# Kernel optimization log

Measured on AMD Instinct MI355X. Metric: run time of the kernel, lower is better.

The kernel has to match this reference:

```python
import jax, jax.numpy as jnp
import numpy as np

B, T, E, H, D = 4, 1024, 1024, 16, 64


def rel_shift(x):
    # x: [B, H, T1, T2] -> Transformer-XL relative shift
    b, h, t1, t2 = x.shape
    x = jnp.pad(x, ((0, 0), (0, 0), (0, 0), (1, 0)))  # pad zeros on left of last dim
    x = x.reshape(b, h, t2 + 1, t1)[:, :, 1:]
    return x.reshape(b, h, t1, t2)


def setup_inputs() -> dict:
    key = jax.random.key(0)
    ks = jax.random.split(key, 9)
    s = 0.02
    return {
        "x": jax.random.normal(ks[0], (B, T, E), jnp.float32),
        "pos": jax.random.normal(ks[1], (1, T, E), jnp.float32),
        "Wq": jax.random.normal(ks[2], (E, H, D), jnp.float32) * s,
        "Wk": jax.random.normal(ks[3], (E, H, D), jnp.float32) * s,
        "Wv": jax.random.normal(ks[4], (E, H, D), jnp.float32) * s,
        "Wr": jax.random.normal(ks[5], (E, H, D), jnp.float32) * s,
        "r_w_bias": jax.random.normal(ks[6], (1, H, 1, D), jnp.float32) * s,
        "r_r_bias": jax.random.normal(ks[7], (1, H, 1, D), jnp.float32) * s,
        "merge_W": jax.random.normal(ks[8], (E, E), jnp.float32) * s,
        "merge_b": jnp.zeros((E,), jnp.float32),
    }


def reference(x, pos, Wq, Wk, Wv, Wr, r_w_bias, r_r_bias, merge_W, merge_b):
    d = Wq.shape[-1]
    scale = d ** -0.5
    # per-head linear projections via einsum (MultiHeadLinear)
    q = jnp.einsum('bte,ehd->bhtd', x, Wq) * scale   # [B,H,T,D]
    k = jnp.einsum('bte,ehd->bhtd', x, Wk)           # [B,H,T,D]
    v = jnp.einsum('bte,ehd->bhtd', x, Wv)           # [B,H,T,D]
    r = jnp.einsum('upe,ehd->uhpd', pos, Wr)[0]      # [H,P,D], P == T

    # content logits: (q + u) . k
    content_logits = jnp.einsum('bhtd,bhsd->bhts', q + r_w_bias, k)
    # relative logits: (q + v_bias) . rel_keys, then rel_shift
    relative_logits = jnp.einsum('bhtd,hpd->bhtp', q + r_r_bias, r)
    relative_logits = rel_shift(relative_logits)

    logits = content_logits + relative_logits        # [B,H,T,T]
    weights = jax.nn.softmax(logits, axis=-1)
    # attend and merge heads: [B,T,H,D] -> [B,T,E]
    attended = jnp.einsum('bhts,bhsd->bthd', weights, v).reshape(x.shape[0], x.shape[1], -1)
    return attended @ merge_W + merge_b
```

## Files before the change

kernel.cpp:

```cpp
#include <hip/hip_runtime.h>
#include <hip/hip_bf16.h>

#define BB 4
#define TT 1024
#define EE 1024
#define HH 16
#define DD 64

typedef unsigned short ushort_t;
typedef unsigned int uint_t;
typedef __attribute__((ext_vector_type(8))) short short8;
typedef __attribute__((ext_vector_type(4))) float f32x4;

__device__ __forceinline__ ushort_t f2bf(float f) {
  uint_t u = __float_as_uint(f);
  u += 0x7fffu + ((u >> 16) & 1u);
  return (ushort_t)(u >> 16);
}
__device__ __forceinline__ float bf2f(ushort_t s) {
  return __uint_as_float(((uint_t)s) << 16);
}

__device__ __forceinline__ void gload16(const ushort_t* src, ushort_t* dst) {
  __builtin_amdgcn_global_load_lds(
      (const __attribute__((address_space(1))) void*)src,
      (__attribute__((address_space(3))) void*)dst, 16, 0, 0);
}

__global__ void __launch_bounds__(256) conv_flat(
    const float* __restrict__ in, ushort_t* __restrict__ out, int n) {
  int i = (blockIdx.x * 256 + threadIdx.x) * 8;
  if (i >= n) return;
  float4 a = *(const float4*)(in + i);
  float4 b = *(const float4*)(in + i + 4);
  uint4 o;
  o.x = (uint_t)f2bf(a.x) | ((uint_t)f2bf(a.y) << 16);
  o.y = (uint_t)f2bf(a.z) | ((uint_t)f2bf(a.w) << 16);
  o.z = (uint_t)f2bf(b.x) | ((uint_t)f2bf(b.y) << 16);
  o.w = (uint_t)f2bf(b.z) | ((uint_t)f2bf(b.w) << 16);
  *(uint4*)(out + i) = o;
}

__global__ void __launch_bounds__(256) trans_conv(
    const float* __restrict__ W, ushort_t* __restrict__ Oh,
    ushort_t* __restrict__ Ol, int has_lo) {
  __shared__ float Ts[64][65];
  const int n0 = blockIdx.x * 64, k0 = blockIdx.y * 64;
  const int t = threadIdx.x;
  const int r = t >> 2, cs = (t & 3) * 16;
  const float* src = W + (size_t)(k0 + r) * 1024 + n0 + cs;
  #pragma unroll
  for (int e = 0; e < 16; e += 4) {
    float4 v4 = *(const float4*)(src + e);
    Ts[r][cs + e] = v4.x; Ts[r][cs + e + 1] = v4.y;
    Ts[r][cs + e + 2] = v4.z; Ts[r][cs + e + 3] = v4.w;
  }
  __syncthreads();
  ushort_t hb[16], lb[16];
  #pragma unroll
  for (int e = 0; e < 16; e++) {
    float v = Ts[cs + e][r];
    hb[e] = f2bf(v);
    lb[e] = f2bf(v - bf2f(hb[e]));
  }
  ushort_t* dh = Oh + (size_t)(n0 + r) * 1024 + k0 + cs;
  *(uint4*)dh = *(const uint4*)hb;
  *(uint4*)(dh + 8) = *(const uint4*)(hb + 8);
  if (has_lo) {
    ushort_t* dl = Ol + (size_t)(n0 + r) * 1024 + k0 + cs;
    *(uint4*)dl = *(const uint4*)lb;
    *(uint4*)(dl + 8) = *(const uint4*)(lb + 8);
  }
}

__global__ void __launch_bounds__(256) mfma_gemm_proj(
    const ushort_t* __restrict__ A,
    const ushort_t* __restrict__ B0, const ushort_t* __restrict__ B1,
    const ushort_t* __restrict__ B2,
    ushort_t* __restrict__ o_qu, ushort_t* __restrict__ o_qv,
    ushort_t* __restrict__ o_k, ushort_t* __restrict__ o_v,
    const float* __restrict__ bias_u, const float* __restrict__ bias_v,
    int mode) {
  __shared__ ushort_t sA[2][128 * 32];
  __shared__ ushort_t sB[2][128 * 32];
  const int tid = threadIdx.x;
  const int w = tid >> 6, lane = tid & 63, g = lane >> 4, cl = lane & 15;
  const int wr = w >> 1, wc = w & 1;

  int widx, n0l;
  const ushort_t* Bt;
  if (mode == 0) {
    widx = blockIdx.x >> 3;
    n0l = (blockIdx.x & 7) * 128;
    Bt = (widx == 0) ? B0 : ((widx == 1) ? B1 : B2);
  } else {
    widx = 3;
    n0l = blockIdx.x * 128;
    Bt = B0;
  }
  const int m0 = blockIdx.y * 128;

  f32x4 acc[4][4];
  #pragma unroll
  for (int fi = 0; fi < 4; fi++)
    #pragma unroll
    for (int fj = 0; fj < 4; fj++) acc[fi][fj] = (f32x4){0.f, 0.f, 0.f, 0.f};

  auto STAGE = [&](int buf, int t) {
    const int k0b = t * 64;
    #pragma unroll
    for (int i = 0; i < 2; i++) {
      int cb = w * 128 + i * 64;
      int c = cb + lane;
      const char* sa = (const char*)A + (size_t)(m0 + (c >> 2)) * 2048 + k0b + (c & 3) * 16;
      gload16((const ushort_t*)sa, &sA[buf][cb * 8]);
      const char* sb = (const char*)Bt + (size_t)(n0l + (c >> 2)) * 2048 + k0b + (c & 3) * 16;
      gload16((const ushort_t*)sb, &sB[buf][cb * 8]);
    }
  };

  STAGE(0, 0);
  __syncthreads();
  int cur = 0;
  for (int t = 0; t < 32; t++) {
    if (t + 1 < 32) STAGE(cur ^ 1, t + 1);
    short8 af[4], bfr[4];
    #pragma unroll
    for (int f = 0; f < 4; f++) {
      af[f] = *(const short8*)&sA[cur][(wr * 64 + f * 16 + cl) * 32 + g * 8];
      bfr[f] = *(const short8*)&sB[cur][(wc * 64 + f * 16 + cl) * 32 + g * 8];
    }
    #pragma unroll
    for (int fi = 0; fi < 4; fi++)
      #pragma unroll
      for (int fj = 0; fj < 4; fj++)
        acc[fi][fj] = __builtin_amdgcn_mfma_f32_16x16x32_bf16(af[fi], bfr[fj], acc[fi][fj], 0, 0, 0);
    __syncthreads();
    cur ^= 1;
  }

  #pragma unroll
  for (int fi = 0; fi < 4; fi++)
    #pragma unroll
    for (int fj = 0; fj < 4; fj++)
      #pragma unroll
      for (int reg = 0; reg < 4; reg++) {
        int m = m0 + wr * 64 + fi * 16 + 4 * g + reg;
        int n = n0l + wc * 64 + fj * 16 + cl;
        float val = acc[fi][fj][reg];
        int h = n >> 6, d = n & 63;
        if (mode == 0) {
          int b = m >> 10, tt = m & 1023;
          size_t idx = (((size_t)(b * HH + h)) * TT + tt) * DD + d;
          if (widx == 0) {
            float s = val * 0.125f;
            o_qu[idx] = f2bf(s + bias_u[n]);
            o_qv[idx] = f2bf(s + bias_v[n]);
          } else if (widx == 1) {
            o_k[idx] = f2bf(val);
          } else {
            o_v[idx] = f2bf(val);
          }
        } else {
          size_t idx = ((size_t)h * TT + m) * DD + d;
          o_qu[idx] = f2bf(val);
        }
      }
}

__global__ void __launch_bounds__(256) mfma_gemm_merge(
    const ushort_t* __restrict__ Ah, const ushort_t* __restrict__ Al,
    const ushort_t* __restrict__ Bh, const ushort_t* __restrict__ Bl,
    const float* __restrict__ bias, float* __restrict__ out) {
  __shared__ ushort_t sAh[2][128 * 32], sAl[2][128 * 32];
  __shared__ ushort_t sBh[2][128 * 32], sBl[2][128 * 32];
  const int tid = threadIdx.x;
  const int w = tid >> 6, lane = tid & 63, g = lane >> 4, cl = lane & 15;
  const int wr = w >> 1, wc = w & 1;
  const int n0l = blockIdx.x * 128;
  const int m0 = blockIdx.y * 128;

  f32x4 acc[4][4];
  #pragma unroll
  for (int fi = 0; fi < 4; fi++)
    #pragma unroll
    for (int fj = 0; fj < 4; fj++) acc[fi][fj] = (f32x4){0.f, 0.f, 0.f, 0.f};

  auto STAGE = [&](int buf, int t) {
    const int k0b = t * 64;
    #pragma unroll
    for (int i = 0; i < 2; i++) {
      int cb = w * 128 + i * 64;
      int c = cb + lane;
      size_t offA = (size_t)(m0 + (c >> 2)) * 2048 + k0b + (c & 3) * 16;
      size_t offB = (size_t)(n0l + (c >> 2)) * 2048 + k0b + (c & 3) * 16;
      gload16((const ushort_t*)((const char*)Ah + offA), &sAh[buf][cb * 8]);
      gload16((const ushort_t*)((const char*)Al + offA), &sAl[buf][cb * 8]);
      gload16((const ushort_t*)((const char*)Bh + offB), &sBh[buf][cb * 8]);
      gload16((const ushort_t*)((const char*)Bl + offB), &sBl[buf][cb * 8]);
    }
  };

  STAGE(0, 0);
  __syncthreads();
  int cur = 0;
  for (int t = 0; t < 32; t++) {
    if (t + 1 < 32) STAGE(cur ^ 1, t + 1);
    short8 ah[4], al[4], bh[4], bl[4];
    #pragma unroll
    for (int f = 0; f < 4; f++) {
      int ra = (wr * 64 + f * 16 + cl) * 32 + g * 8;
      int rb = (wc * 64 + f * 16 + cl) * 32 + g * 8;
      ah[f] = *(const short8*)&sAh[cur][ra];
      al[f] = *(const short8*)&sAl[cur][ra];
      bh[f] = *(const short8*)&sBh[cur][rb];
      bl[f] = *(const short8*)&sBl[cur][rb];
    }
    #pragma unroll
    for (int fi = 0; fi < 4; fi++)
      #pragma unroll
      for (int fj = 0; fj < 4; fj++) {
        acc[fi][fj] = __builtin_amdgcn_mfma_f32_16x16x32_bf16(ah[fi], bh[fj], acc[fi][fj], 0, 0, 0);
        acc[fi][fj] = __builtin_amdgcn_mfma_f32_16x16x32_bf16(al[fi], bh[fj], acc[fi][fj], 0, 0, 0);
        acc[fi][fj] = __builtin_amdgcn_mfma_f32_16x16x32_bf16(ah[fi], bl[fj], acc[fi][fj], 0, 0, 0);
      }
    __syncthreads();
    cur ^= 1;
  }

  #pragma unroll
  for (int fi = 0; fi < 4; fi++)
    #pragma unroll
    for (int fj = 0; fj < 4; fj++)
      #pragma unroll
      for (int reg = 0; reg < 4; reg++) {
        int m = m0 + wr * 64 + fi * 16 + 4 * g + reg;
        int n = n0l + wc * 64 + fj * 16 + cl;
        out[(size_t)m * 1024 + n] = acc[fi][fj][reg] + bias[n];
      }
}

__device__ __forceinline__ void stage8(ushort_t* region, const ushort_t* grow0,
                                       int r0, int lane, int rmax) {
  int flat16 = r0 * 8 + lane;
  int row = flat16 >> 3;
  int ch = flat16 & 7;
  int gr = row > rmax ? rmax : row;
  const ushort_t* src = grow0 + (size_t)gr * 64 + ((((ch << 4) ^ ((row & 7) << 4))) >> 1);
  gload16(src, region + r0 * 64);
}

__device__ __forceinline__ short8 ldsw(const ushort_t* base, int row, int offB) {
  const char* p = (const char*)base + row * 128 + (offB ^ ((row & 7) << 4));
  return *(const short8*)p;
}

__global__ void __launch_bounds__(256, 3) attn_mfma_kernel(
    const ushort_t* __restrict__ qu_g, const ushort_t* __restrict__ qv_g,
    const ushort_t* __restrict__ k_g, const ushort_t* __restrict__ v_g,
    const ushort_t* __restrict__ r_g,
    ushort_t* __restrict__ att_h, ushort_t* __restrict__ att_l)
{
    __shared__ ushort_t sK[2][64 * 64];
    __shared__ ushort_t sVt[2][64 * 72];
    __shared__ ushort_t sG[4][2304];

    const int tid = threadIdx.x;
    const int w = tid >> 6;
    const int lane = tid & 63;
    const int g = lane >> 4;
    const int cl = lane & 15;

    const int i0 = blockIdx.x * 64;
    const int h = blockIdx.y;
    const int b = blockIdx.z;
    const size_t base_bh = ((size_t)(b * HH + h)) * TT * DD;
    const ushort_t* rh = r_g + (size_t)h * TT * DD;

    ushort_t* Gw = sG[w];
    ushort_t* Pb = sG[w];

    const int qrow = i0 + 16 * w + cl;
    const ushort_t* qup = qu_g + base_bh + (size_t)qrow * 64;
    short8 aQ0 = *(const short8*)(qup + 8 * g);
    short8 aQ1 = *(const short8*)(qup + 32 + 8 * g);
    const ushort_t* qv1p = qv_g + base_bh + (size_t)qrow * 64;
    short8 aV0 = *(const short8*)(qv1p + 8 * g);
    short8 aV1 = *(const short8*)(qv1p + 32 + 8 * g);
    int r2row = qrow + 1; if (r2row > 1023) r2row = 1023;
    const ushort_t* qv2p = qv_g + base_bh + (size_t)r2row * 64;
    short8 aV0s = *(const short8*)(qv2p + 8 * g);
    short8 aV1s = *(const short8*)(qv2p + 32 + 8 * g);

    auto STAGEK = [&](int bufi, int jt16) {
      const ushort_t* kb = k_g + base_bh + (size_t)(jt16 * 64) * 64;
      stage8(sK[bufi], kb, 16 * w, lane, 63);
      stage8(sK[bufi], kb, 16 * w + 8, lane, 63);
    };
    const int vjj = tid & 63;
    const int vd0 = (tid >> 6) * 16;
    auto LOADV = [&](int jt16, short8& v0, short8& v1) {
      const ushort_t* vs = v_g + base_bh + (size_t)(jt16 * 64 + vjj) * 64 + vd0;
      v0 = *(const short8*)vs;
      v1 = *(const short8*)(vs + 8);
    };
    auto WRITEV = [&](int bufi, short8 v0, short8 v1) {
      ushort_t* dst = &sVt[bufi][0];
      #pragma unroll
      for (int e = 0; e < 8; e++) dst[(vd0 + e) * 72 + vjj] = (ushort_t)v0[e];
      #pragma unroll
      for (int e = 0; e < 8; e++) dst[(vd0 + 8 + e) * 72 + vjj] = (ushort_t)v1[e];
    };

    f32x4 Oa[4];
    #pragma unroll
    for (int q = 0; q < 4; q++) Oa[q] = (f32x4){0.f, 0.f, 0.f, 0.f};
    float mrun[4] = {-1e30f, -1e30f, -1e30f, -1e30f};
    float lrun[4] = {0.f, 0.f, 0.f, 0.f};

    STAGEK(0, 0);
    short8 pv0, pv1;
    LOADV(0, pv0, pv1);
    WRITEV(0, pv0, pv1);
    __syncthreads();
    int cur = 0;

    for (int jt16 = 0; jt16 < 16; jt16++) {
        const int j0 = jt16 * 64;
        const int dji = j0 - i0;
        ushort_t* Gw2 = Gw + ((dji == 0) ? 64 * 18 : 0);

        f32x4 sacc[4];
        #pragma unroll
        for (int jt = 0; jt < 4; jt++) sacc[jt] = (f32x4){0.f, 0.f, 0.f, 0.f};
        __builtin_amdgcn_s_setprio(1);
        #pragma unroll
        for (int jt = 0; jt < 4; jt++) {
            int krow = jt * 16 + cl;
            short8 b0 = ldsw(sK[cur], krow, 16 * g);
            short8 b1 = ldsw(sK[cur], krow, 64 + 16 * g);
            sacc[jt] = __builtin_amdgcn_mfma_f32_16x16x32_bf16(aQ0, b0, sacc[jt], 0, 0, 0);
            sacc[jt] = __builtin_amdgcn_mfma_f32_16x16x32_bf16(aQ1, b1, sacc[jt], 0, 0, 0);
        }
        __builtin_amdgcn_s_setprio(0);

        if (dji <= 0) {
            int cbase = 960 + dji;
            int nsub = (dji == 0) ? 4 : 8;
            for (int sub = 0; sub < nsub; sub++) {
                int m = sub * 16 + cl;
                int rr = cbase + m;
                rr = rr < 0 ? 0 : (rr > 1023 ? 1023 : rr);
                const ushort_t* rp = rh + (size_t)rr * 64 + 8 * g;
                f32x4 gacc = (f32x4){0.f, 0.f, 0.f, 0.f};
                gacc = __builtin_amdgcn_mfma_f32_16x16x32_bf16(aV0, *(const short8*)rp, gacc, 0, 0, 0);
                gacc = __builtin_amdgcn_mfma_f32_16x16x32_bf16(aV1, *(const short8*)(rp + 32), gacc, 0, 0, 0);
                *(uint_t*)(Gw + m * 18 + 4 * g) =
                    (uint_t)f2bf(gacc[0]) | ((uint_t)f2bf(gacc[1]) << 16);
                *(uint_t*)(Gw + m * 18 + 4 * g + 2) =
                    (uint_t)f2bf(gacc[2]) | ((uint_t)f2bf(gacc[3]) << 16);
            }
        }
        if (dji >= 0) {
            int cb2 = dji - 65; if (cb2 < 0) cb2 = 0;
            int nsub = (dji == 0) ? 4 : 8;
            for (int sub = 0; sub < nsub; sub++) {
                int m = sub * 16 + cl;
                int rr = cb2 + m;
                rr = rr > 1023 ? 1023 : rr;
                const ushort_t* rp = rh + (size_t)rr * 64 + 8 * g;
                f32x4 gacc = (f32x4){0.f, 0.f, 0.f, 0.f};
                gacc = __builtin_amdgcn_mfma_f32_16x16x32_bf16(aV0s, *(const short8*)rp, gacc, 0, 0, 0);
                gacc = __builtin_amdgcn_mfma_f32_16x16x32_bf16(aV1s, *(const short8*)(rp + 32), gacc, 0, 0, 0);
                *(uint_t*)(Gw2 + m * 18 + 4 * g) =
                    (uint_t)f2bf(gacc[0]) | ((uint_t)f2bf(gacc[1]) << 16);
                *(uint_t*)(Gw2 + m * 18 + 4 * g + 2) =
                    (uint_t)f2bf(gacc[2]) | ((uint_t)f2bf(gacc[3]) << 16);
            }
        }

        if (jt16 + 1 < 16) {
            STAGEK(cur ^ 1, jt16 + 1);
            LOADV(jt16 + 1, pv0, pv1);
        }

        if (dji <= 0) {
            int lim = 63 - dji;
            #pragma unroll
            for (int jt = 0; jt < 4; jt++)
                #pragma unroll
                for (int reg = 0; reg < 4; reg++) {
                    int m1 = 63 + jt * 16 + cl - 16 * w - 4 * g - reg;
                    if (m1 <= lim) sacc[jt][reg] += bf2f(Gw[m1 * 18 + 4 * g + reg]);
                }
        }
        if (dji >= 0) {
            int cb2 = dji - 65; if (cb2 < 0) cb2 = 0;
            #pragma unroll
            for (int jt = 0; jt < 4; jt++)
                #pragma unroll
                for (int reg = 0; reg < 4; reg++) {
                    int dlt = dji + jt * 16 + cl - 16 * w - 4 * g - reg;
                    if (dlt >= 2) sacc[jt][reg] += bf2f(Gw2[(dlt - 2 - cb2) * 18 + 4 * g + reg]);
                }
        }

        #pragma unroll
        for (int reg = 0; reg < 4; reg++) {
            float tmax = fmaxf(fmaxf(sacc[0][reg], sacc[1][reg]),
                               fmaxf(sacc[2][reg], sacc[3][reg]));
            #pragma unroll
            for (int msk = 1; msk <= 8; msk <<= 1) tmax = fmaxf(tmax, __shfl_xor(tmax, msk));
            float mnew = fmaxf(mrun[reg], tmax);
            float sc = __expf(mrun[reg] - mnew);
            mrun[reg] = mnew;
            float psum = 0.f;
            #pragma unroll
            for (int jt = 0; jt < 4; jt++) {
                float p = __expf(sacc[jt][reg] - mnew);
                psum += p;
                Pb[(4 * g + reg) * 72 + jt * 16 + cl] = f2bf(p);
            }
            #pragma unroll
            for (int msk = 1; msk <= 8; msk <<= 1) psum += __shfl_xor(psum, msk);
            lrun[reg] = lrun[reg] * sc + psum;
            #pragma unroll
            for (int q = 0; q < 4; q++) Oa[q][reg] *= sc;
        }

        __builtin_amdgcn_s_setprio(1);
        #pragma unroll
        for (int kk = 0; kk < 2; kk++) {
            short8 aP = *(const short8*)((const char*)Pb + cl * 144 + 64 * kk + 16 * g);
            #pragma unroll
            for (int q = 0; q < 4; q++) {
                int vrow = q * 16 + cl;
                short8 bV = *(const short8*)((const char*)&sVt[cur][0] + vrow * 144 + 64 * kk + 16 * g);
                Oa[q] = __builtin_amdgcn_mfma_f32_16x16x32_bf16(aP, bV, Oa[q], 0, 0, 0);
            }
        }
        __builtin_amdgcn_s_setprio(0);

        if (jt16 + 1 < 16) WRITEV(cur ^ 1, pv0, pv1);

        __syncthreads();
        cur ^= 1;
    }

    float inv[4];
    #pragma unroll
    for (int reg = 0; reg < 4; reg++) inv[reg] = 1.f / lrun[reg];
    #pragma unroll
    for (int q = 0; q < 4; q++)
        #pragma unroll
        for (int reg = 0; reg < 4; reg++) {
            int i = i0 + 16 * w + 4 * g + reg;
            int d = q * 16 + cl;
            float val = Oa[q][reg] * inv[reg];
            ushort_t hi = f2bf(val);
            ushort_t lo = f2bf(val - bf2f(hi));
            size_t oi = (((size_t)(b * TT + i)) * HH + h) * DD + d;
            att_h[oi] = hi;
            att_l[oi] = lo;
        }
}

extern "C" void kernel_launch(void* const* d_in, const int* in_sizes, int n_in,
                              void* d_out, int out_size, void* d_ws, size_t ws_size,
                              hipStream_t stream) {
    const float* x    = (const float*)d_in[0];
    const float* pos  = (const float*)d_in[1];
    const float* Wq   = (const float*)d_in[2];
    const float* Wk   = (const float*)d_in[3];
    const float* Wv   = (const float*)d_in[4];
    const float* Wr   = (const float*)d_in[5];
    const float* ub   = (const float*)d_in[6];
    const float* vb   = (const float*)d_in[7];
    const float* mW   = (const float*)d_in[8];
    const float* mb   = (const float*)d_in[9];
    float* out = (float*)d_out;

    const size_t M1 = 1u << 20;
    ushort_t* ws = (ushort_t*)d_ws;
    ushort_t* xb   = ws;
    ushort_t* posb = ws + 4 * M1;
    ushort_t* wqt  = ws + 5 * M1;
    ushort_t* wkt  = ws + 6 * M1;
    ushort_t* wvt  = ws + 7 * M1;
    ushort_t* wrt  = ws + 8 * M1;
    ushort_t* wmh  = ws + 9 * M1;
    ushort_t* wml  = ws + 10 * M1;
    ushort_t* qu_g = ws + 11 * M1;
    ushort_t* qv_g = ws + 15 * M1;
    ushort_t* k_g  = ws + 19 * M1;
    ushort_t* v_g  = ws + 23 * M1;
    ushort_t* r_g  = ws + 27 * M1;
    ushort_t* ath  = ws + 28 * M1;
    ushort_t* atl  = ws + 32 * M1;

    dim3 blk(256);

    hipLaunchKernelGGL(conv_flat, dim3(2048), blk, 0, stream, x, xb, 4194304);
    hipLaunchKernelGGL(conv_flat, dim3(512), blk, 0, stream, pos, posb, 1048576);
    dim3 gtr(16, 16);
    hipLaunchKernelGGL(trans_conv, gtr, blk, 0, stream, Wq, wqt, (ushort_t*)nullptr, 0);
    hipLaunchKernelGGL(trans_conv, gtr, blk, 0, stream, Wk, wkt, (ushort_t*)nullptr, 0);
    hipLaunchKernelGGL(trans_conv, gtr, blk, 0, stream, Wv, wvt, (ushort_t*)nullptr, 0);
    hipLaunchKernelGGL(trans_conv, gtr, blk, 0, stream, Wr, wrt, (ushort_t*)nullptr, 0);
    hipLaunchKernelGGL(trans_conv, gtr, blk, 0, stream, mW, wmh, wml, 1);

    hipLaunchKernelGGL(mfma_gemm_proj, dim3(24, 32), blk, 0, stream,
                       xb, wqt, wkt, wvt, qu_g, qv_g, k_g, v_g, ub, vb, 0);
    hipLaunchKernelGGL(mfma_gemm_proj, dim3(8, 8), blk, 0, stream,
                       posb, wrt, wrt, wrt, r_g, r_g, r_g, r_g, ub, vb, 1);

    hipLaunchKernelGGL(attn_mfma_kernel, dim3(TT / 64, HH, BB), blk, 0, stream,
                       qu_g, qv_g, k_g, v_g, r_g, ath, atl);

    hipLaunchKernelGGL(mfma_gemm_merge, dim3(8, 32), blk, 0, stream,
                       ath, atl, wmh, wml, mb, out);
}
```

Before: 333.3 us.

## Store V transposed and stage it via async LDS loads; remap attention blocks per XCD

The projection GEMM now writes V in a [B,H,D,T] transposed layout. The attention kernel can then stage V tiles with the same swizzled global_load_lds path as K, instead of register loads followed by a scalar transposing LDS write. The attention grid is remapped so that all query tiles of the same (b,h) land on the same XCD, which improves L2 reuse of K/V/R. The four weight transposes are also merged into one launch. The risks are strided, uncoalesced scalar stores of V in the projection epilogue and a block mapping that assumes exactly 1024 blocks.

```diff
diff --git a/kernel.cpp b/kernel.cpp
--- a/kernel.cpp
+++ b/kernel.cpp
@@ -41,9 +41,18 @@
   *(uint4*)(out + i) = o;
 }
 
-__global__ void __launch_bounds__(256) trans_conv(
-    const float* __restrict__ W, ushort_t* __restrict__ Oh,
-    ushort_t* __restrict__ Ol, int has_lo) {
+__global__ void __launch_bounds__(256) trans_conv4(
+    const float* __restrict__ W0, const float* __restrict__ W1,
+    const float* __restrict__ W2, const float* __restrict__ W3,
+    ushort_t* __restrict__ O0, ushort_t* __restrict__ O1,
+    ushort_t* __restrict__ O2, ushort_t* __restrict__ O3) {
+  const float* W; ushort_t* Oh;
+  switch (blockIdx.z) {
+    case 0: W = W0; Oh = O0; break;
+    case 1: W = W1; Oh = O1; break;
+    case 2: W = W2; Oh = O2; break;
+    default: W = W3; Oh = O3; break;
+  }
   __shared__ float Ts[64][65];
   const int n0 = blockIdx.x * 64, k0 = blockIdx.y * 64;
   const int t = threadIdx.x;
@@ -56,6 +65,29 @@
     Ts[r][cs + e + 2] = v4.z; Ts[r][cs + e + 3] = v4.w;
   }
   __syncthreads();
+  ushort_t hb[16];
+  #pragma unroll
+  for (int e = 0; e < 16; e++) hb[e] = f2bf(Ts[cs + e][r]);
+  ushort_t* dh = Oh + (size_t)(n0 + r) * 1024 + k0 + cs;
+  *(uint4*)dh = *(const uint4*)hb;
+  *(uint4*)(dh + 8) = *(const uint4*)(hb + 8);
+}
+
+__global__ void __launch_bounds__(256) trans_conv(
+    const float* __restrict__ W, ushort_t* __restrict__ Oh,
+    ushort_t* __restrict__ Ol) {
+  __shared__ float Ts[64][65];
+  const int n0 = blockIdx.x * 64, k0 = blockIdx.y * 64;
+  const int t = threadIdx.x;
+  const int r = t >> 2, cs = (t & 3) * 16;
+  const float* src = W + (size_t)(k0 + r) * 1024 + n0 + cs;
+  #pragma unroll
+  for (int e = 0; e < 16; e += 4) {
+    float4 v4 = *(const float4*)(src + e);
+    Ts[r][cs + e] = v4.x; Ts[r][cs + e + 1] = v4.y;
+    Ts[r][cs + e + 2] = v4.z; Ts[r][cs + e + 3] = v4.w;
+  }
+  __syncthreads();
   ushort_t hb[16], lb[16];
   #pragma unroll
   for (int e = 0; e < 16; e++) {
@@ -66,11 +98,9 @@
   ushort_t* dh = Oh + (size_t)(n0 + r) * 1024 + k0 + cs;
   *(uint4*)dh = *(const uint4*)hb;
   *(uint4*)(dh + 8) = *(const uint4*)(hb + 8);
-  if (has_lo) {
-    ushort_t* dl = Ol + (size_t)(n0 + r) * 1024 + k0 + cs;
-    *(uint4*)dl = *(const uint4*)lb;
-    *(uint4*)(dl + 8) = *(const uint4*)(lb + 8);
-  }
+  ushort_t* dl = Ol + (size_t)(n0 + r) * 1024 + k0 + cs;
+  *(uint4*)dl = *(const uint4*)lb;
+  *(uint4*)(dl + 8) = *(const uint4*)(lb + 8);
 }
 
 __global__ void __launch_bounds__(256) mfma_gemm_proj(
@@ -151,14 +181,16 @@
         int h = n >> 6, d = n & 63;
         if (mode == 0) {
           int b = m >> 10, tt = m & 1023;
-          size_t idx = (((size_t)(b * HH + h)) * TT + tt) * DD + d;
           if (widx == 0) {
+            size_t idx = (((size_t)(b * HH + h)) * TT + tt) * DD + d;
             float s = val * 0.125f;
             o_qu[idx] = f2bf(s + bias_u[n]);
             o_qv[idx] = f2bf(s + bias_v[n]);
           } else if (widx == 1) {
+            size_t idx = (((size_t)(b * HH + h)) * TT + tt) * DD + d;
             o_k[idx] = f2bf(val);
           } else {
+            size_t idx = (((size_t)(b * HH + h)) * DD + d) * TT + tt;
             o_v[idx] = f2bf(val);
           }
         } else {
@@ -240,13 +272,12 @@
       }
 }
 
-__device__ __forceinline__ void stage8(ushort_t* region, const ushort_t* grow0,
-                                       int r0, int lane, int rmax) {
+__device__ __forceinline__ void stage8s(ushort_t* region, const ushort_t* grow0,
+                                        int rstride, int r0, int lane) {
   int flat16 = r0 * 8 + lane;
   int row = flat16 >> 3;
   int ch = flat16 & 7;
-  int gr = row > rmax ? rmax : row;
-  const ushort_t* src = grow0 + (size_t)gr * 64 + ((((ch << 4) ^ ((row & 7) << 4))) >> 1);
+  const ushort_t* src = grow0 + (size_t)row * rstride + ((((ch << 4) ^ ((row & 7) << 4))) >> 1);
   gload16(src, region + r0 * 64);
 }
 
@@ -257,12 +288,12 @@
 
 __global__ void __launch_bounds__(256, 3) attn_mfma_kernel(
     const ushort_t* __restrict__ qu_g, const ushort_t* __restrict__ qv_g,
-    const ushort_t* __restrict__ k_g, const ushort_t* __restrict__ v_g,
+    const ushort_t* __restrict__ k_g, const ushort_t* __restrict__ vt_g,
     const ushort_t* __restrict__ r_g,
     ushort_t* __restrict__ att_h, ushort_t* __restrict__ att_l)
 {
     __shared__ ushort_t sK[2][64 * 64];
-    __shared__ ushort_t sVt[2][64 * 72];
+    __shared__ ushort_t sVt[2][64 * 64];
     __shared__ ushort_t sG[4][2304];
 
     const int tid = threadIdx.x;
@@ -271,9 +302,12 @@
     const int g = lane >> 4;
     const int cl = lane & 15;
 
-    const int i0 = blockIdx.x * 64;
-    const int h = blockIdx.y;
-    const int b = blockIdx.z;
+    const int lid = blockIdx.x + 16 * blockIdx.y + 256 * blockIdx.z;
+    const int xcd = lid & 7, seq = lid >> 3;
+    const int bhg = xcd * 8 + (seq >> 4);
+    const int i0 = (seq & 15) * 64;
+    const int h = bhg & 15;
+    const int b = bhg >> 4;
     const size_t base_bh = ((size_t)(b * HH + h)) * TT * DD;
     const ushort_t* rh = r_g + (size_t)h * TT * DD;
 
@@ -292,24 +326,13 @@
     short8 aV0s = *(const short8*)(qv2p + 8 * g);
     short8 aV1s = *(const short8*)(qv2p + 32 + 8 * g);
 
-    auto STAGEK = [&](int bufi, int jt16) {
+    auto STAGE = [&](int bufi, int jt16) {
       const ushort_t* kb = k_g + base_bh + (size_t)(jt16 * 64) * 64;
-      stage8(sK[bufi], kb, 16 * w, lane, 63);
-      stage8(sK[bufi], kb, 16 * w + 8, lane, 63);
-    };
-    const int vjj = tid & 63;
-    const int vd0 = (tid >> 6) * 16;
-    auto LOADV = [&](int jt16, short8& v0, short8& v1) {
-      const ushort_t* vs = v_g + base_bh + (size_t)(jt16 * 64 + vjj) * 64 + vd0;
-      v0 = *(const short8*)vs;
-      v1 = *(const short8*)(vs + 8);
-    };
-    auto WRITEV = [&](int bufi, short8 v0, short8 v1) {
-      ushort_t* dst = &sVt[bufi][0];
-      #pragma unroll
-      for (int e = 0; e < 8; e++) dst[(vd0 + e) * 72 + vjj] = (ushort_t)v0[e];
-      #pragma unroll
-      for (int e = 0; e < 8; e++) dst[(vd0 + 8 + e) * 72 + vjj] = (ushort_t)v1[e];
+      stage8s(sK[bufi], kb, 64, 16 * w, lane);
+      stage8s(sK[bufi], kb, 64, 16 * w + 8, lane);
+      const ushort_t* vtb = vt_g + base_bh + (size_t)(jt16 * 64);
+      stage8s(sVt[bufi], vtb, 1024, 16 * w, lane);
+      stage8s(sVt[bufi], vtb, 1024, 16 * w + 8, lane);
     };
 
     f32x4 Oa[4];
@@ -318,10 +341,7 @@
     float mrun[4] = {-1e30f, -1e30f, -1e30f, -1e30f};
     float lrun[4] = {0.f, 0.f, 0.f, 0.f};
 
-    STAGEK(0, 0);
-    short8 pv0, pv1;
-    LOADV(0, pv0, pv1);
-    WRITEV(0, pv0, pv1);
+    STAGE(0, 0);
     __syncthreads();
     int cur = 0;
 
@@ -379,10 +399,7 @@
             }
         }
 
-        if (jt16 + 1 < 16) {
-            STAGEK(cur ^ 1, jt16 + 1);
-            LOADV(jt16 + 1, pv0, pv1);
-        }
+        if (jt16 + 1 < 16) STAGE(cur ^ 1, jt16 + 1);
 
         if (dji <= 0) {
             int lim = 63 - dji;
@@ -434,14 +451,11 @@
             short8 aP = *(const short8*)((const char*)Pb + cl * 144 + 64 * kk + 16 * g);
             #pragma unroll
             for (int q = 0; q < 4; q++) {
-                int vrow = q * 16 + cl;
-                short8 bV = *(const short8*)((const char*)&sVt[cur][0] + vrow * 144 + 64 * kk + 16 * g);
+                short8 bV = ldsw(sVt[cur], q * 16 + cl, kk * 64 + 16 * g);
                 Oa[q] = __builtin_amdgcn_mfma_f32_16x16x32_bf16(aP, bV, Oa[q], 0, 0, 0);
             }
         }
         __builtin_amdgcn_s_setprio(0);
-
-        if (jt16 + 1 < 16) WRITEV(cur ^ 1, pv0, pv1);
 
         __syncthreads();
         cur ^= 1;
@@ -493,7 +507,7 @@
     ushort_t* qu_g = ws + 11 * M1;
     ushort_t* qv_g = ws + 15 * M1;
     ushort_t* k_g  = ws + 19 * M1;
-    ushort_t* v_g  = ws + 23 * M1;
+    ushort_t* vt_g = ws + 23 * M1;
     ushort_t* r_g  = ws + 27 * M1;
     ushort_t* ath  = ws + 28 * M1;
     ushort_t* atl  = ws + 32 * M1;
@@ -502,20 +516,17 @@
 
     hipLaunchKernelGGL(conv_flat, dim3(2048), blk, 0, stream, x, xb, 4194304);
     hipLaunchKernelGGL(conv_flat, dim3(512), blk, 0, stream, pos, posb, 1048576);
-    dim3 gtr(16, 16);
-    hipLaunchKernelGGL(trans_conv, gtr, blk, 0, stream, Wq, wqt, (ushort_t*)nullptr, 0);
-    hipLaunchKernelGGL(trans_conv, gtr, blk, 0, stream, Wk, wkt, (ushort_t*)nullptr, 0);
-    hipLaunchKernelGGL(trans_conv, gtr, blk, 0, stream, Wv, wvt, (ushort_t*)nullptr, 0);
-    hipLaunchKernelGGL(trans_conv, gtr, blk, 0, stream, Wr, wrt, (ushort_t*)nullptr, 0);
-    hipLaunchKernelGGL(trans_conv, gtr, blk, 0, stream, mW, wmh, wml, 1);
+    hipLaunchKernelGGL(trans_conv4, dim3(16, 16, 4), blk, 0, stream,
+                       Wq, Wk, Wv, Wr, wqt, wkt, wvt, wrt);
+    hipLaunchKernelGGL(trans_conv, dim3(16, 16), blk, 0, stream, mW, wmh, wml);
 
     hipLaunchKernelGGL(mfma_gemm_proj, dim3(24, 32), blk, 0, stream,
-                       xb, wqt, wkt, wvt, qu_g, qv_g, k_g, v_g, ub, vb, 0);
+                       xb, wqt, wkt, wvt, qu_g, qv_g, k_g, vt_g, ub, vb, 0);
     hipLaunchKernelGGL(mfma_gemm_proj, dim3(8, 8), blk, 0, stream,
                        posb, wrt, wrt, wrt, r_g, r_g, r_g, r_g, ub, vb, 1);
 
     hipLaunchKernelGGL(attn_mfma_kernel, dim3(TT / 64, HH, BB), blk, 0, stream,
-                       qu_g, qv_g, k_g, v_g, r_g, ath, atl);
+                       qu_g, qv_g, k_g, vt_g, r_g, ath, atl);
 
     hipLaunchKernelGGL(mfma_gemm_merge, dim3(8, 32), blk, 0, stream,
                        ath, atl, wmh, wml, mb, out);
```

Measured after the change: 349.8 us. 1.05x slower.
